# Performance work log

Measured on AMD Instinct MI355X. Metric: run time of the kernel, lower is better.

## Reference

```python
import jax, jax.numpy as jnp
import numpy as np

H = 16
D_MODEL = 1024
D_K = D_MODEL // H
B, S = 4, 2048


def setup_inputs() -> dict:
    key = jax.random.key(0)
    ks = jax.random.split(key, 12)
    scale = 1.0 / np.sqrt(D_MODEL)
    inp = {
        "query": jax.random.normal(ks[0], (B, S, D_MODEL), jnp.float32),
        "key_in": jax.random.normal(ks[1], (B, S, D_MODEL), jnp.float32),
        "value": jax.random.normal(ks[2], (B, S, D_MODEL), jnp.float32),
        "mask": jax.random.randint(ks[3], (B, 1, S, S), 0, 2, jnp.int32),
    }
    # 4 Linear(d_model, d_model) layers: Wq, Wk, Wv, Wo (+ biases)
    names = ["q", "k", "v", "o"]
    for i, n in enumerate(names):
        inp[f"W{n}"] = jax.random.normal(ks[4 + i], (D_MODEL, D_MODEL), jnp.float32) * scale
        inp[f"b{n}"] = jax.random.normal(ks[8 + i], (D_MODEL,), jnp.float32) * scale
    return inp


def reference(query, key_in, value, mask, Wq, bq, Wk, bk, Wv, bv, Wo, bo):
    # Linear projections then split heads: [B,S,D] -> [B,H,S,Dk]
    def proj(x, W, b):
        y = jnp.einsum("bsd,ed->bse", x, W) + b  # torch Linear: x @ W.T + b
        return y.reshape(B, S, H, D_K).transpose(0, 2, 1, 3)

    q = proj(query, Wq, bq)
    k = proj(key_in, Wk, bk)
    v = proj(value, Wv, bv)

    scores = jnp.einsum("bhqd,bhkd->bhqk", q, k) / jnp.sqrt(jnp.float32(D_K))
    scores = jnp.where(mask == 0, jnp.float32(-1e9), scores)
    p_attn = jax.nn.softmax(scores, axis=-1)
    # dropout is identity in eval mode
    x = jnp.einsum("bhqk,bhkd->bhqd", p_attn, v)
    x = x.transpose(0, 2, 1, 3).reshape(B, S, D_MODEL)
    return jnp.einsum("bsd,ed->bse", x, Wo) + bo
```

## Files before the change

### kernel.cpp

```cpp
#include <hip/hip_runtime.h>
#include <hip/hip_bf16.h>

typedef __bf16 bf16_t;
typedef __attribute__((ext_vector_type(8))) __bf16 bf16x8;
typedef __attribute__((ext_vector_type(4))) __bf16 bf16x4;
typedef __attribute__((ext_vector_type(4))) float f32x4;

#define GAS __attribute__((address_space(1)))
#define LAS __attribute__((address_space(3)))

__device__ __forceinline__ void async_copy16(const bf16_t* g, bf16_t* l) {
    __builtin_amdgcn_global_load_lds((const GAS void*)g, (LAS void*)l, 16, 0, 0);
}

__global__ __launch_bounds__(256) void convert_kernel(
    const float* __restrict__ src, bf16_t* __restrict__ dst, int n)
{
    int i = (blockIdx.x * 256 + threadIdx.x) * 8;
    if (i >= n) return;
    f32x4 f0 = *(const f32x4*)(src + i);
    f32x4 f1 = *(const f32x4*)(src + i + 4);
    bf16x8 v;
#pragma unroll
    for (int j = 0; j < 4; j++) { v[j] = (bf16_t)f0[j]; v[4 + j] = (bf16_t)f1[j]; }
    *(bf16x8*)&dst[i] = v;
}

struct WConvArgs {
    const float *s0, *s1, *s2, *s3;
    bf16_t *d0, *d1, *d2, *d3;
};

__global__ __launch_bounds__(256) void wconv_kernel(WConvArgs a)
{
    const int seg = blockIdx.y;
    const float* src = seg == 0 ? a.s0 : seg == 1 ? a.s1 : seg == 2 ? a.s2 : a.s3;
    bf16_t*     dst = seg == 0 ? a.d0 : seg == 1 ? a.d1 : seg == 2 ? a.d2 : a.d3;
    int i = (blockIdx.x * 256 + threadIdx.x) * 8;
    f32x4 f0 = *(const f32x4*)(src + i);
    f32x4 f1 = *(const f32x4*)(src + i + 4);
    bf16x8 v;
#pragma unroll
    for (int j = 0; j < 4; j++) { v[j] = (bf16_t)f0[j]; v[4 + j] = (bf16_t)f1[j]; }
    *(bf16x8*)&dst[i] = v;
}

__global__ __launch_bounds__(256) void pack_mask_kernel(
    const int* __restrict__ mask, unsigned long long* __restrict__ out)
{
    int i = blockIdx.x * 256 + threadIdx.x;
    unsigned long long bits = __ballot(mask[i] != 0);
    if ((threadIdx.x & 63) == 0) out[i >> 6] = bits;
}

template<int MODE>
__global__ __launch_bounds__(256, 2) void gemm_nt(
    const bf16_t* __restrict__ A, const bf16_t* __restrict__ W,
    const float* __restrict__ bias, void* __restrict__ out_, float oscale)
{
    __shared__ __align__(16) bf16_t Als[128 * 32];
    __shared__ __align__(16) bf16_t Bls[128 * 32];

    const int tid  = threadIdx.x;
    const int wave = tid >> 6, lane = tid & 63;
    const int quad = lane >> 4, lq = lane & 15;
    const int wm = wave >> 1, wn = wave & 1;
    const int tm = blockIdx.x * 128, tn = blockIdx.y * 128;
    const int K = 1024;

    const bf16_t* gA0 = A + (size_t)(tm + wave * 32 + (lane >> 2)) * K + (lane & 3) * 8;
    const bf16_t* gA1 = gA0 + (size_t)16 * K;
    const bf16_t* gB0 = W + (size_t)(tn + wave * 32 + (lane >> 2)) * K + (lane & 3) * 8;
    const bf16_t* gB1 = gB0 + (size_t)16 * K;
    bf16_t* lA0 = &Als[(wave * 32) * 32];
    bf16_t* lA1 = &Als[(wave * 32 + 16) * 32];
    bf16_t* lB0 = &Bls[(wave * 32) * 32];
    bf16_t* lB1 = &Bls[(wave * 32 + 16) * 32];

    f32x4 acc[4][4] = {};

    for (int k0 = 0; k0 < K; k0 += 32) {
        __syncthreads();
        async_copy16(gA0, lA0);
        async_copy16(gA1, lA1);
        async_copy16(gB0, lB0);
        async_copy16(gB1, lB1);
        gA0 += 32; gA1 += 32; gB0 += 32; gB1 += 32;
        __syncthreads();

        bf16x8 af[4], bfr[4];
#pragma unroll
        for (int i = 0; i < 4; i++) {
            af[i]  = *(const bf16x8*)&Als[(wm * 64 + i * 16 + lq) * 32 + quad * 8];
            bfr[i] = *(const bf16x8*)&Bls[(wn * 64 + i * 16 + lq) * 32 + quad * 8];
        }
#pragma unroll
        for (int i = 0; i < 4; i++)
#pragma unroll
            for (int j = 0; j < 4; j++) {
                if (MODE == 2)
                    acc[i][j] = __builtin_amdgcn_mfma_f32_16x16x32_bf16(bfr[j], af[i], acc[i][j], 0, 0, 0);
                else
                    acc[i][j] = __builtin_amdgcn_mfma_f32_16x16x32_bf16(af[i], bfr[j], acc[i][j], 0, 0, 0);
            }
    }

    float* outf = (float*)out_;
    bf16_t* outb = (bf16_t*)out_;
#pragma unroll
    for (int i = 0; i < 4; i++)
#pragma unroll
        for (int j = 0; j < 4; j++)
#pragma unroll
            for (int r = 0; r < 4; r++) {
                float v = acc[i][j][r];
                if (MODE == 0) {
                    int row = tm + wm * 64 + i * 16 + quad * 4 + r;
                    int col = tn + wn * 64 + j * 16 + lq;
                    outf[(size_t)row * 1024 + col] = (v + bias[col]) * oscale;
                } else if (MODE == 1) {
                    int row = tm + wm * 64 + i * 16 + quad * 4 + r;
                    int col = tn + wn * 64 + j * 16 + lq;
                    v = (v + bias[col]) * oscale;
                    int b = row >> 11, s = row & 2047;
                    int h = col >> 6,  dk = col & 63;
                    outb[(((size_t)(b * 16 + h) * 2048 + s) << 6) + dk] = (bf16_t)v;
                } else {
                    int n = tn + wn * 64 + j * 16 + quad * 4 + r;
                    int m = tm + wm * 64 + i * 16 + lq;
                    v = (v + bias[n]) * oscale;
                    int b = m >> 11, s = m & 2047;
                    int h = n >> 6,  dk = n & 63;
                    outb[((size_t)((b * 16 + h) * 64 + dk) << 11) + s] = (bf16_t)v;
                }
            }
}

#define LDK 72
#define LDV 72
#define LDP 72

__global__ __launch_bounds__(256, 2) void attn_kernel(
    const bf16_t* __restrict__ Q, const bf16_t* __restrict__ Kh,
    const bf16_t* __restrict__ Vt, const unsigned int* __restrict__ mp,
    bf16_t* __restrict__ X)
{
    __shared__ __align__(16) bf16_t Kls[64 * LDK];
    __shared__ __align__(16) bf16_t Vls[64 * LDV];
    __shared__ __align__(16) bf16_t Pls[4][32 * LDP];

    const int tid  = threadIdx.x;
    const int wave = tid >> 6, lane = tid & 63;
    const int quad = lane >> 4, lq = lane & 15;
    const int xr8  = lq & 8;
    const int bh = blockIdx.y;
    const int b  = bh >> 4, h = bh & 15;
    const int qwv = blockIdx.x * 128 + wave * 32;

    bf16x8 qf[2][2];
#pragma unroll
    for (int qs = 0; qs < 2; qs++) {
        const bf16_t* qptr = Q + ((size_t)bh * 2048 + qwv + qs * 16 + lq) * 64 + quad * 8;
        qf[qs][0] = *(const bf16x8*)qptr;
        qf[qs][1] = *(const bf16x8*)(qptr + 32);
    }

    f32x4 o[2][4] = {};
    f32x4 ls[2] = {};

    const int sr = tid >> 3, sc = tid & 7;
    const bf16_t* gK0 = Kh + ((size_t)bh * 2048 + sr) * 64 + sc * 8;
    const bf16_t* gK1 = gK0 + 32 * 64;
    const bf16_t* gV0 = Vt + ((size_t)bh * 64 + sr) * 2048 + sc * 8;
    const bf16_t* gV1 = gV0 + 32 * 2048;
    const int swc = (sc * 8) ^ (sr & 8);
    bf16_t* lK0 = &Kls[sr * LDK + swc];
    bf16_t* lK1 = &Kls[(sr + 32) * LDK + swc];
    bf16_t* lV0 = &Vls[sr * LDV + swc];
    bf16_t* lV1 = &Vls[(sr + 32) * LDV + swc];

    const unsigned int* mr0 = mp + ((size_t)(b << 11) + qwv + lq) * 64;

    bf16x8 ks0 = *(const bf16x8*)gK0, ks1 = *(const bf16x8*)gK1;
    bf16x8 vs0 = *(const bf16x8*)gV0, vs1 = *(const bf16x8*)gV1;

    for (int kt = 0; kt < 32; kt++) {
        __syncthreads();
        *(bf16x8*)lK0 = ks0; *(bf16x8*)lK1 = ks1;
        *(bf16x8*)lV0 = vs0; *(bf16x8*)lV1 = vs1;
        __syncthreads();
        if (kt < 31) {
            gK0 += 4096; gK1 += 4096; gV0 += 64; gV1 += 64;
            ks0 = *(const bf16x8*)gK0; ks1 = *(const bf16x8*)gK1;
            vs0 = *(const bf16x8*)gV0; vs1 = *(const bf16x8*)gV1;
        }
        unsigned int w[2][2];
        w[0][0] = mr0[2 * kt];        w[0][1] = mr0[2 * kt + 1];
        w[1][0] = mr0[2 * kt + 1024]; w[1][1] = mr0[2 * kt + 1025];

        bf16_t* pb = &Pls[wave][0];
#pragma unroll
        for (int nt = 0; nt < 2; nt++) {
        }
#pragma unroll
        for (int nt = 0; nt < 4; nt++) {
            const bf16_t* krow = &Kls[(nt * 16 + lq) * LDK];
            bf16x8 kf0 = *(const bf16x8*)(krow + ((quad * 8) ^ xr8));
            bf16x8 kf1 = *(const bf16x8*)(krow + 32 + ((quad * 8) ^ xr8));
#pragma unroll
            for (int qs = 0; qs < 2; qs++) {
                f32x4 z = {};
                z = __builtin_amdgcn_mfma_f32_16x16x32_bf16(kf0, qf[qs][0], z, 0, 0, 0);
                z = __builtin_amdgcn_mfma_f32_16x16x32_bf16(kf1, qf[qs][1], z, 0, 0, 0);
                unsigned int wq = w[qs][nt >> 1] >> ((nt & 1) * 16 + quad * 4);
                bf16x4 pk;
#pragma unroll
                for (int r = 0; r < 4; r++) {
                    float sv = ((wq >> r) & 1) ? z[r] : -1e9f;
                    float p = __expf(sv);
                    ls[qs][r] += p;
                    pk[r] = (bf16_t)p;
                }
                *(bf16x4*)&pb[(qs * 16 + lq) * LDP + nt * 16 + quad * 4] = pk;
            }
        }

#pragma unroll
        for (int c = 0; c < 2; c++) {
            bf16x8 pf0 = *(const bf16x8*)&pb[lq * LDP + c * 32 + quad * 8];
            bf16x8 pf1 = *(const bf16x8*)&pb[(16 + lq) * LDP + c * 32 + quad * 8];
#pragma unroll
            for (int dt = 0; dt < 4; dt++) {
                bf16x8 vf = *(const bf16x8*)&Vls[(dt * 16 + lq) * LDV +
                                                 (c * 32 + ((quad * 8) ^ xr8))];
                o[0][dt] = __builtin_amdgcn_mfma_f32_16x16x32_bf16(pf0, vf, o[0][dt], 0, 0, 0);
                o[1][dt] = __builtin_amdgcn_mfma_f32_16x16x32_bf16(pf1, vf, o[1][dt], 0, 0, 0);
            }
        }
    }

#pragma unroll
    for (int qs = 0; qs < 2; qs++) {
        float l = (ls[qs][0] + ls[qs][1]) + (ls[qs][2] + ls[qs][3]);
        l += __shfl_xor(l, 16);
        l += __shfl_xor(l, 32);
        float rl[4];
#pragma unroll
        for (int r = 0; r < 4; r++) {
            float lv = __shfl(l, quad * 4 + r);
            rl[r] = (lv > 0.f) ? 1.0f / lv : 0.f;
        }
#pragma unroll
        for (int dt = 0; dt < 4; dt++)
#pragma unroll
            for (int r = 0; r < 4; r++) {
                int qrow = qwv + qs * 16 + quad * 4 + r;
                X[((size_t)(b * 2048) + qrow) * 1024 + h * 64 + dt * 16 + lq] =
                    (bf16_t)(o[qs][dt][r] * rl[r]);
            }
    }
}

extern "C" void kernel_launch(void* const* d_in, const int* in_sizes, int n_in,
                              void* d_out, int out_size, void* d_ws, size_t ws_size,
                              hipStream_t stream)
{
    const float* query  = (const float*)d_in[0];
    const float* key_in = (const float*)d_in[1];
    const float* value  = (const float*)d_in[2];
    const int*   mask   = (const int*)d_in[3];

    char* ws = (char*)d_ws;
    const size_t SZ  = (size_t)8192 * 1024 * 2;
    const size_t MPK = (size_t)2 * 1024 * 1024;
    const size_t WSZ = (size_t)1024 * 1024 * 2;
    bf16_t* C   = (bf16_t*)(ws);
    bf16_t* Qb  = (bf16_t*)(ws + SZ);
    bf16_t* Kb  = (bf16_t*)(ws + 2 * SZ);
    bf16_t* Vtb = (bf16_t*)(ws + 3 * SZ);
    unsigned long long* mpack = (unsigned long long*)(ws + 4 * SZ);
    bf16_t* Wc[4];
    for (int i = 0; i < 4; i++)
        Wc[i] = (bf16_t*)(ws + 4 * SZ + MPK + i * WSZ);

    const size_t NEED = 4 * SZ + MPK + 4 * WSZ;
    if (ws_size < NEED) return;

    const int NACT = 8192 * 1024;
    WConvArgs wa = { (const float*)d_in[4], (const float*)d_in[6],
                     (const float*)d_in[8], (const float*)d_in[10],
                     Wc[0], Wc[1], Wc[2], Wc[3] };
    wconv_kernel<<<dim3(512, 4), 256, 0, stream>>>(wa);
    pack_mask_kernel<<<65536, 256, 0, stream>>>(mask, mpack);

    dim3 gg(64, 8);
    convert_kernel<<<4096, 256, 0, stream>>>(query, C, NACT);
    gemm_nt<1><<<gg, 256, 0, stream>>>(C, Wc[0], (const float*)d_in[5], Qb, 0.125f);
    convert_kernel<<<4096, 256, 0, stream>>>(key_in, C, NACT);
    gemm_nt<1><<<gg, 256, 0, stream>>>(C, Wc[1], (const float*)d_in[7], Kb, 1.0f);
    convert_kernel<<<4096, 256, 0, stream>>>(value, C, NACT);
    gemm_nt<2><<<gg, 256, 0, stream>>>(C, Wc[2], (const float*)d_in[9], Vtb, 1.0f);

    attn_kernel<<<dim3(16, 64), 256, 0, stream>>>(Qb, Kb, Vtb,
                                                  (const unsigned int*)mpack, C);
    gemm_nt<0><<<gg, 256, 0, stream>>>(C, Wc[3], (const float*)d_in[11], d_out, 1.0f);
}
```

Baseline: 437.5 us.

## Batch QKV conversion and projections into single launches; drop attention LDS swizzle

When the workspace is large enough, the three activation conversions run as one launch and the Q, K and V projections run as one 3D-grid GEMM over separate buffers. This removes serial launches and lets the three projections fill the GPU together. The attention kernel drops the XOR swizzle on K/V shared memory and shrinks the P row padding from 72 to 68, which may change LDS bank conflicts. The old serial path is kept as a fallback when the workspace is smaller.

```diff
diff --git a/kernel.cpp b/kernel.cpp
--- a/kernel.cpp
+++ b/kernel.cpp
@@ -36,6 +36,25 @@
     const int seg = blockIdx.y;
     const float* src = seg == 0 ? a.s0 : seg == 1 ? a.s1 : seg == 2 ? a.s2 : a.s3;
     bf16_t*     dst = seg == 0 ? a.d0 : seg == 1 ? a.d1 : seg == 2 ? a.d2 : a.d3;
+    int i = (blockIdx.x * 256 + threadIdx.x) * 8;
+    f32x4 f0 = *(const f32x4*)(src + i);
+    f32x4 f1 = *(const f32x4*)(src + i + 4);
+    bf16x8 v;
+#pragma unroll
+    for (int j = 0; j < 4; j++) { v[j] = (bf16_t)f0[j]; v[4 + j] = (bf16_t)f1[j]; }
+    *(bf16x8*)&dst[i] = v;
+}
+
+struct AConvArgs {
+    const float *s0, *s1, *s2;
+    bf16_t *d0, *d1, *d2;
+};
+
+__global__ __launch_bounds__(256) void aconv_kernel(AConvArgs a)
+{
+    const int seg = blockIdx.y;
+    const float* src = seg == 0 ? a.s0 : seg == 1 ? a.s1 : a.s2;
+    bf16_t*     dst = seg == 0 ? a.d0 : seg == 1 ? a.d1 : a.d2;
     int i = (blockIdx.x * 256 + threadIdx.x) * 8;
     f32x4 f0 = *(const f32x4*)(src + i);
     f32x4 f1 = *(const f32x4*)(src + i + 4);
@@ -136,9 +155,102 @@
             }
 }
 
+struct QKV3Args {
+    const bf16_t *A0, *A1, *A2;
+    const bf16_t *W0, *W1, *W2;
+    const float  *b0, *b1, *b2;
+    bf16_t *o0, *o1, *o2;
+};
+
+__global__ __launch_bounds__(256, 2) void qkv3_gemm(QKV3Args g)
+{
+    __shared__ __align__(16) bf16_t Als[128 * 32];
+    __shared__ __align__(16) bf16_t Bls[128 * 32];
+
+    const int z = blockIdx.z;
+    const bf16_t* A    = z == 0 ? g.A0 : z == 1 ? g.A1 : g.A2;
+    const bf16_t* W    = z == 0 ? g.W0 : z == 1 ? g.W1 : g.W2;
+    const float*  bias = z == 0 ? g.b0 : z == 1 ? g.b1 : g.b2;
+    bf16_t*       outb = z == 0 ? g.o0 : z == 1 ? g.o1 : g.o2;
+    const float oscale = (z == 0) ? 0.125f : 1.0f;
+    const bool  vmode  = (z == 2);
+
+    const int tid  = threadIdx.x;
+    const int wave = tid >> 6, lane = tid & 63;
+    const int quad = lane >> 4, lq = lane & 15;
+    const int wm = wave >> 1, wn = wave & 1;
+    const int tm = blockIdx.x * 128, tn = blockIdx.y * 128;
+    const int K = 1024;
+
+    const bf16_t* gA0 = A + (size_t)(tm + wave * 32 + (lane >> 2)) * K + (lane & 3) * 8;
+    const bf16_t* gA1 = gA0 + (size_t)16 * K;
+    const bf16_t* gB0 = W + (size_t)(tn + wave * 32 + (lane >> 2)) * K + (lane & 3) * 8;
+    const bf16_t* gB1 = gB0 + (size_t)16 * K;
+    bf16_t* lA0 = &Als[(wave * 32) * 32];
+    bf16_t* lA1 = &Als[(wave * 32 + 16) * 32];
+    bf16_t* lB0 = &Bls[(wave * 32) * 32];
+    bf16_t* lB1 = &Bls[(wave * 32 + 16) * 32];
+
+    f32x4 acc[4][4] = {};
+
+    for (int k0 = 0; k0 < K; k0 += 32) {
+        __syncthreads();
+        async_copy16(gA0, lA0);
+        async_copy16(gA1, lA1);
+        async_copy16(gB0, lB0);
+        async_copy16(gB1, lB1);
+        gA0 += 32; gA1 += 32; gB0 += 32; gB1 += 32;
+        __syncthreads();
+
+        bf16x8 af[4], bfr[4];
+#pragma unroll
+        for (int i = 0; i < 4; i++) {
+            af[i]  = *(const bf16x8*)&Als[(wm * 64 + i * 16 + lq) * 32 + quad * 8];
+            bfr[i] = *(const bf16x8*)&Bls[(wn * 64 + i * 16 + lq) * 32 + quad * 8];
+        }
+        if (vmode) {
+#pragma unroll
+            for (int i = 0; i < 4; i++)
+#pragma unroll
+                for (int j = 0; j < 4; j++)
+                    acc[i][j] = __builtin_amdgcn_mfma_f32_16x16x32_bf16(bfr[j], af[i], acc[i][j], 0, 0, 0);
+        } else {
+#pragma unroll
+            for (int i = 0; i < 4; i++)
+#pragma unroll
+                for (int j = 0; j < 4; j++)
+                    acc[i][j] = __builtin_amdgcn_mfma_f32_16x16x32_bf16(af[i], bfr[j], acc[i][j], 0, 0, 0);
+        }
+    }
+
+#pragma unroll
+    for (int i = 0; i < 4; i++)
+#pragma unroll
+        for (int j = 0; j < 4; j++)
+#pragma unroll
+            for (int r = 0; r < 4; r++) {
+                float v = acc[i][j][r];
+                if (!vmode) {
+                    int row = tm + wm * 64 + i * 16 + quad * 4 + r;
+                    int col = tn + wn * 64 + j * 16 + lq;
+                    v = (v + bias[col]) * oscale;
+                    int b = row >> 11, s = row & 2047;
+                    int h = col >> 6,  dk = col & 63;
+                    outb[(((size_t)(b * 16 + h) * 2048 + s) << 6) + dk] = (bf16_t)v;
+                } else {
+                    int n = tn + wn * 64 + j * 16 + quad * 4 + r;
+                    int m = tm + wm * 64 + i * 16 + lq;
+                    v = v + bias[n];
+                    int b = m >> 11, s = m & 2047;
+                    int h = n >> 6,  dk = n & 63;
+                    outb[((size_t)((b * 16 + h) * 64 + dk) << 11) + s] = (bf16_t)v;
+                }
+            }
+}
+
 #define LDK 72
 #define LDV 72
-#define LDP 72
+#define LDP 68
 
 __global__ __launch_bounds__(256, 2) void attn_kernel(
     const bf16_t* __restrict__ Q, const bf16_t* __restrict__ Kh,
@@ -152,7 +264,6 @@
     const int tid  = threadIdx.x;
     const int wave = tid >> 6, lane = tid & 63;
     const int quad = lane >> 4, lq = lane & 15;
-    const int xr8  = lq & 8;
     const int bh = blockIdx.y;
     const int b  = bh >> 4, h = bh & 15;
     const int qwv = blockIdx.x * 128 + wave * 32;
@@ -173,11 +284,10 @@
     const bf16_t* gK1 = gK0 + 32 * 64;
     const bf16_t* gV0 = Vt + ((size_t)bh * 64 + sr) * 2048 + sc * 8;
     const bf16_t* gV1 = gV0 + 32 * 2048;
-    const int swc = (sc * 8) ^ (sr & 8);
-    bf16_t* lK0 = &Kls[sr * LDK + swc];
-    bf16_t* lK1 = &Kls[(sr + 32) * LDK + swc];
-    bf16_t* lV0 = &Vls[sr * LDV + swc];
-    bf16_t* lV1 = &Vls[(sr + 32) * LDV + swc];
+    bf16_t* lK0 = &Kls[sr * LDK + sc * 8];
+    bf16_t* lK1 = &Kls[(sr + 32) * LDK + sc * 8];
+    bf16_t* lV0 = &Vls[sr * LDV + sc * 8];
+    bf16_t* lV1 = &Vls[(sr + 32) * LDV + sc * 8];
 
     const unsigned int* mr0 = mp + ((size_t)(b << 11) + qwv + lq) * 64;
 
@@ -200,13 +310,10 @@
 
         bf16_t* pb = &Pls[wave][0];
 #pragma unroll
-        for (int nt = 0; nt < 2; nt++) {
-        }
-#pragma unroll
         for (int nt = 0; nt < 4; nt++) {
             const bf16_t* krow = &Kls[(nt * 16 + lq) * LDK];
-            bf16x8 kf0 = *(const bf16x8*)(krow + ((quad * 8) ^ xr8));
-            bf16x8 kf1 = *(const bf16x8*)(krow + 32 + ((quad * 8) ^ xr8));
+            bf16x8 kf0 = *(const bf16x8*)(krow + quad * 8);
+            bf16x8 kf1 = *(const bf16x8*)(krow + 32 + quad * 8);
 #pragma unroll
             for (int qs = 0; qs < 2; qs++) {
                 f32x4 z = {};
@@ -231,8 +338,7 @@
             bf16x8 pf1 = *(const bf16x8*)&pb[(16 + lq) * LDP + c * 32 + quad * 8];
 #pragma unroll
             for (int dt = 0; dt < 4; dt++) {
-                bf16x8 vf = *(const bf16x8*)&Vls[(dt * 16 + lq) * LDV +
-                                                 (c * 32 + ((quad * 8) ^ xr8))];
+                bf16x8 vf = *(const bf16x8*)&Vls[(dt * 16 + lq) * LDV + c * 32 + quad * 8];
                 o[0][dt] = __builtin_amdgcn_mfma_f32_16x16x32_bf16(pf0, vf, o[0][dt], 0, 0, 0);
                 o[1][dt] = __builtin_amdgcn_mfma_f32_16x16x32_bf16(pf1, vf, o[1][dt], 0, 0, 0);
             }
@@ -274,34 +380,68 @@
     const size_t SZ  = (size_t)8192 * 1024 * 2;
     const size_t MPK = (size_t)2 * 1024 * 1024;
     const size_t WSZ = (size_t)1024 * 1024 * 2;
-    bf16_t* C   = (bf16_t*)(ws);
-    bf16_t* Qb  = (bf16_t*)(ws + SZ);
-    bf16_t* Kb  = (bf16_t*)(ws + 2 * SZ);
-    bf16_t* Vtb = (bf16_t*)(ws + 3 * SZ);
-    unsigned long long* mpack = (unsigned long long*)(ws + 4 * SZ);
-    bf16_t* Wc[4];
-    for (int i = 0; i < 4; i++)
-        Wc[i] = (bf16_t*)(ws + 4 * SZ + MPK + i * WSZ);
-
-    const size_t NEED = 4 * SZ + MPK + 4 * WSZ;
-    if (ws_size < NEED) return;
+    const size_t NEED_FULL = 6 * SZ + MPK + 4 * WSZ;
+    const size_t NEED_SER  = 4 * SZ + MPK + 4 * WSZ;
 
     const int NACT = 8192 * 1024;
-    WConvArgs wa = { (const float*)d_in[4], (const float*)d_in[6],
-                     (const float*)d_in[8], (const float*)d_in[10],
-                     Wc[0], Wc[1], Wc[2], Wc[3] };
-    wconv_kernel<<<dim3(512, 4), 256, 0, stream>>>(wa);
-    pack_mask_kernel<<<65536, 256, 0, stream>>>(mask, mpack);
-
-    dim3 gg(64, 8);
-    convert_kernel<<<4096, 256, 0, stream>>>(query, C, NACT);
-    gemm_nt<1><<<gg, 256, 0, stream>>>(C, Wc[0], (const float*)d_in[5], Qb, 0.125f);
-    convert_kernel<<<4096, 256, 0, stream>>>(key_in, C, NACT);
-    gemm_nt<1><<<gg, 256, 0, stream>>>(C, Wc[1], (const float*)d_in[7], Kb, 1.0f);
-    convert_kernel<<<4096, 256, 0, stream>>>(value, C, NACT);
-    gemm_nt<2><<<gg, 256, 0, stream>>>(C, Wc[2], (const float*)d_in[9], Vtb, 1.0f);
-
-    attn_kernel<<<dim3(16, 64), 256, 0, stream>>>(Qb, Kb, Vtb,
-                                                  (const unsigned int*)mpack, C);
-    gemm_nt<0><<<gg, 256, 0, stream>>>(C, Wc[3], (const float*)d_in[11], d_out, 1.0f);
-}
+
+    if (ws_size >= NEED_FULL) {
+        bf16_t* A0  = (bf16_t*)(ws);
+        bf16_t* A1  = (bf16_t*)(ws + SZ);
+        bf16_t* A2  = (bf16_t*)(ws + 2 * SZ);
+        bf16_t* Qb  = (bf16_t*)(ws + 3 * SZ);
+        bf16_t* Kb  = (bf16_t*)(ws + 4 * SZ);
+        bf16_t* Vtb = (bf16_t*)(ws + 5 * SZ);
+        unsigned long long* mpack = (unsigned long long*)(ws + 6 * SZ);
+        bf16_t* Wc[4];
+        for (int i = 0; i < 4; i++)
+            Wc[i] = (bf16_t*)(ws + 6 * SZ + MPK + i * WSZ);
+
+        WConvArgs wa = { (const float*)d_in[4], (const float*)d_in[6],
+                         (const float*)d_in[8], (const float*)d_in[10],
+                         Wc[0], Wc[1], Wc[2], Wc[3] };
+        wconv_kernel<<<dim3(512, 4), 256, 0, stream>>>(wa);
+        pack_mask_kernel<<<65536, 256, 0, stream>>>(mask, mpack);
+
+        AConvArgs aa = { query, key_in, value, A0, A1, A2 };
+        aconv_kernel<<<dim3(4096, 3), 256, 0, stream>>>(aa);
+
+        QKV3Args qa = { A0, A1, A2, Wc[0], Wc[1], Wc[2],
+                        (const float*)d_in[5], (const float*)d_in[7],
+                        (const float*)d_in[9], Qb, Kb, Vtb };
+        qkv3_gemm<<<dim3(64, 8, 3), 256, 0, stream>>>(qa);
+
+        bf16_t* X = A0;
+        attn_kernel<<<dim3(16, 64), 256, 0, stream>>>(Qb, Kb, Vtb,
+                                                      (const unsigned int*)mpack, X);
+        gemm_nt<0><<<dim3(64, 8), 256, 0, stream>>>(X, Wc[3], (const float*)d_in[11],
+                                                    d_out, 1.0f);
+    } else if (ws_size >= NEED_SER) {
+        bf16_t* C   = (bf16_t*)(ws);
+        bf16_t* Qb  = (bf16_t*)(ws + SZ);
+        bf16_t* Kb  = (bf16_t*)(ws + 2 * SZ);
+        bf16_t* Vtb = (bf16_t*)(ws + 3 * SZ);
+        unsigned long long* mpack = (unsigned long long*)(ws + 4 * SZ);
+        bf16_t* Wc[4];
+        for (int i = 0; i < 4; i++)
+            Wc[i] = (bf16_t*)(ws + 4 * SZ + MPK + i * WSZ);
+
+        WConvArgs wa = { (const float*)d_in[4], (const float*)d_in[6],
+                         (const float*)d_in[8], (const float*)d_in[10],
+                         Wc[0], Wc[1], Wc[2], Wc[3] };
+        wconv_kernel<<<dim3(512, 4), 256, 0, stream>>>(wa);
+        pack_mask_kernel<<<65536, 256, 0, stream>>>(mask, mpack);
+
+        dim3 gg(64, 8);
+        convert_kernel<<<4096, 256, 0, stream>>>(query, C, NACT);
+        gemm_nt<1><<<gg, 256, 0, stream>>>(C, Wc[0], (const float*)d_in[5], Qb, 0.125f);
+        convert_kernel<<<4096, 256, 0, stream>>>(key_in, C, NACT);
+        gemm_nt<1><<<gg, 256, 0, stream>>>(C, Wc[1], (const float*)d_in[7], Kb, 1.0f);
+        convert_kernel<<<4096, 256, 0, stream>>>(value, C, NACT);
+        gemm_nt<2><<<gg, 256, 0, stream>>>(C, Wc[2], (const float*)d_in[9], Vtb, 1.0f);
+
+        attn_kernel<<<dim3(16, 64), 256, 0, stream>>>(Qb, Kb, Vtb,
+                                                      (const unsigned int*)mpack, C);
+        gemm_nt<0><<<gg, 256, 0, stream>>>(C, Wc[3], (const float*)d_in[11], d_out, 1.0f);
+    }
+}
```

Result: slower. 474.5 us (+8.5%).
